# Optimization experiments

Hardware: AMD Instinct MI355X
Metric: run time of the kernel (lower is better)

Reference implementation:

```python
import jax, jax.numpy as jnp
import numpy as np

D = 128
NUM_GATE = 100000
T = 524288
IDX_MAX = 256


def sinusoid_table(n, d):
    # generate_fixed_embedding for indices 0..n-1, vectorized
    pos = jnp.arange(n, dtype=jnp.float32)[:, None]                      # [n,1]
    div = jnp.exp(jnp.arange(0, d, 2, dtype=jnp.float32)
                  * (-jnp.log(jnp.float32(10000.0)) / d))                # [d/2]
    ang = pos * div                                                      # [n,d/2]
    enc = jnp.zeros((n, d), jnp.float32)
    return enc.at[:, 0::2].set(jnp.sin(ang)).at[:, 1::2].set(jnp.cos(ang))


def setup_inputs() -> dict:
    key = jax.random.key(0)
    ks = jax.random.split(key, 10)
    bound = 1.0 / np.sqrt(3 * D)  # torch Linear default init bound
    return {
        "gate_emb": jax.random.normal(ks[0], (NUM_GATE, D), jnp.float32),
        "edge_emb": jax.random.normal(ks[1], (2, D), jnp.float32),
        "W": jax.random.uniform(ks[2], (D, 3 * D), jnp.float32, -bound, bound),
        "b": jax.random.uniform(ks[3], (D,), jnp.float32, -bound, bound),
        "src_idx": jax.random.randint(ks[4], (T,), 0, IDX_MAX, jnp.int32),
        "src_type": jax.random.randint(ks[5], (T,), 0, 4, jnp.int32),
        "rel": jax.random.randint(ks[6], (T,), 0, 2, jnp.int32),
        "dst_idx": jax.random.randint(ks[7], (T,), 0, IDX_MAX, jnp.int32),
        "dst_type": jax.random.randint(ks[8], (T,), 0, 4, jnp.int32),
        "num_input_nodes": IDX_MAX,
        "num_output_nodes": IDX_MAX,
    }


def reference(gate_emb, edge_emb, W, b, src_idx, src_type, rel, dst_idx,
              dst_type, num_input_nodes, num_output_nodes):
    d = gate_emb.shape[1]
    inp_enc = sinusoid_table(num_input_nodes, d)    # [Ni,d]
    out_enc = sinusoid_table(num_output_nodes, d)   # [No,d]
    ni, no, ng = inp_enc.shape[0], out_enc.shape[0], gate_emb.shape[0]
    # one flat table: [input | output | gate | constant(zeros)]
    table = jnp.concatenate(
        [inp_enc, out_enc, gate_emb, jnp.zeros((1, d), gate_emb.dtype)], axis=0)
    offsets = jnp.array([0, ni, ni + no, ni + no + ng], jnp.int32)

    def node_embed(idx, typ):
        # constant nodes (type 3) ignore idx and map to the zero row
        flat = offsets[typ] + jnp.where(typ == 3, 0, idx)
        return table[flat]                           # [T,d]

    src = node_embed(src_idx, src_type)
    dst = node_embed(dst_idx, dst_type)
    r = edge_emb[rel]                                # [T,d]
    x = jnp.concatenate([src, r, dst], axis=-1)      # [T,3d]
    return x @ W.T + b                               # [T,d]
```

## Files before the change

kernel.cpp:

```cpp
#include <hip/hip_runtime.h>
#include <math.h>

#define DD 128
#define NROWS 769
#define T_TOTAL 524288

typedef float vfloat4 __attribute__((ext_vector_type(4)));


#define WT_OFF    0
#define PSRC_OFF  (3 * DD * DD)
#define PDST_OFF  (PSRC_OFF + NROWS * DD)
#define PREL_OFF  (PDST_OFF + NROWS * DD)

__global__ void transposeW(const float* __restrict__ W, float* __restrict__ Wt) {
    int k = blockIdx.x;
    int j = threadIdx.x;
    Wt[0 * DD * DD + k * DD + j] = W[j * 384 + k];
    Wt[1 * DD * DD + k * DD + j] = W[j * 384 + 128 + k];
    Wt[2 * DD * DD + k * DD + j] = W[j * 384 + 256 + k];
}

__global__ __launch_bounds__(DD) void prep(
    const float* __restrict__ gate_emb, const float* __restrict__ edge_emb,
    const float* __restrict__ b, const float* __restrict__ Wt,
    float* __restrict__ Psrc, float* __restrict__ Pdst,
    float* __restrict__ Prel) {
    __shared__ float row[DD];
    int r = blockIdx.x;
    int j = threadIdx.x;

    if (r < NROWS) {
        float v;
        if (r < 512) {
            int p = r & 255;
            int i = j >> 1;
            float div = expf(-logf(10000.0f) * (2.0f * (float)i) / 128.0f);
            float ang = (float)p * div;
            v = (j & 1) ? cosf(ang) : sinf(ang);
        } else if (r < 768) {
            v = gate_emb[(r - 512) * DD + j];
        } else {
            v = 0.0f;
        }
        row[j] = v;
        __syncthreads();
        const float* Ws = Wt;
        const float* Wd = Wt + 2 * DD * DD;
        float s = 0.0f, d = 0.0f;
#pragma unroll 8
        for (int k = 0; k < DD; ++k) {
            float e = row[k];
            s = fmaf(e, Ws[k * DD + j], s);
            d = fmaf(e, Wd[k * DD + j], d);
        }
        Psrc[r * DD + j] = s;
        Pdst[r * DD + j] = d;
    } else {
        int rr = r - NROWS;
        row[j] = edge_emb[rr * DD + j];
        __syncthreads();
        const float* Wr = Wt + 1 * DD * DD;
        float s = b[j];
#pragma unroll 8
        for (int k = 0; k < DD; ++k) s = fmaf(row[k], Wr[k * DD + j], s);
        Prel[rr * DD + j] = s;
    }
}

__global__ __launch_bounds__(256) void gather_add(
    const int* __restrict__ src_idx, const int* __restrict__ src_type,
    const int* __restrict__ rel, const int* __restrict__ dst_idx,
    const int* __restrict__ dst_type,
    const vfloat4* __restrict__ Psrc, const vfloat4* __restrict__ Pdst,
    const vfloat4* __restrict__ Prel, vfloat4* __restrict__ out) {
    __shared__ int spk[64];
    int tid  = threadIdx.x;
    int lane = tid & 31;
    int grp  = tid >> 5;
    int rowBase = blockIdx.x * 64;

    if (tid < 64) {
        int t = rowBase + tid;
        int s = src_type[t], d = dst_type[t];
        int fs = (s == 3) ? 768 : s * 256 + src_idx[t];
        int fd = (d == 3) ? 768 : d * 256 + dst_idx[t];
        spk[tid] = fs | (fd << 10) | (rel[t] << 20);
    }
    vfloat4 rel0 = Prel[lane];
    vfloat4 rel1 = Prel[32 + lane];
    __syncthreads();

    int pk[8];
#pragma unroll
    for (int i = 0; i < 8; ++i) pk[i] = spk[grp + 8 * i];

    vfloat4 a[8], c[8];
#pragma unroll
    for (int i = 0; i < 8; ++i) a[i] = Psrc[(pk[i] & 1023) * 32 + lane];
#pragma unroll
    for (int i = 0; i < 8; ++i) c[i] = Pdst[((pk[i] >> 10) & 1023) * 32 + lane];

#pragma unroll
    for (int i = 0; i < 8; ++i) {
        vfloat4 o = a[i] + c[i] + ((pk[i] >> 20) ? rel1 : rel0);
        __builtin_nontemporal_store(o, &out[(rowBase + grp + 8 * i) * 32 + lane]);
    }
}

extern "C" void kernel_launch(void* const* d_in, const int* in_sizes, int n_in,
                              void* d_out, int out_size, void* d_ws, size_t ws_size,
                              hipStream_t stream) {
    const float* gate_emb = (const float*)d_in[0];
    const float* edge_emb = (const float*)d_in[1];
    const float* W        = (const float*)d_in[2];
    const float* b        = (const float*)d_in[3];
    const int* src_idx    = (const int*)d_in[4];
    const int* src_type   = (const int*)d_in[5];
    const int* rel        = (const int*)d_in[6];
    const int* dst_idx    = (const int*)d_in[7];
    const int* dst_type   = (const int*)d_in[8];

    float* ws   = (float*)d_ws;
    float* Wt   = ws + WT_OFF;
    float* Psrc = ws + PSRC_OFF;
    float* Pdst = ws + PDST_OFF;
    float* Prel = ws + PREL_OFF;

    transposeW<<<DD, DD, 0, stream>>>(W, Wt);
    prep<<<NROWS + 2, DD, 0, stream>>>(gate_emb, edge_emb, b, Wt,
                                       Psrc, Pdst, Prel);
    gather_add<<<T_TOTAL / 64, 256, 0, stream>>>(
        src_idx, src_type, rel, dst_idx, dst_type,
        (const vfloat4*)Psrc, (const vfloat4*)Pdst, (const vfloat4*)Prel,
        (vfloat4*)d_out);
}
```

Before: 338.7 us.

## Precompute packed gather indices in the transpose kernel, drop shared-memory sync

```diff
diff --git a/kernel.cpp b/kernel.cpp
--- a/kernel.cpp
+++ b/kernel.cpp
@@ -6,19 +6,44 @@
 #define T_TOTAL 524288
 
 typedef float vfloat4 __attribute__((ext_vector_type(4)));
+typedef int   vint4   __attribute__((ext_vector_type(4)));
 
 
 #define WT_OFF    0
 #define PSRC_OFF  (3 * DD * DD)
 #define PDST_OFF  (PSRC_OFF + NROWS * DD)
 #define PREL_OFF  (PDST_OFF + NROWS * DD)
+#define PK_OFF    (PREL_OFF + 2 * DD)
 
-__global__ void transposeW(const float* __restrict__ W, float* __restrict__ Wt) {
-    int k = blockIdx.x;
-    int j = threadIdx.x;
-    Wt[0 * DD * DD + k * DD + j] = W[j * 384 + k];
-    Wt[1 * DD * DD + k * DD + j] = W[j * 384 + 128 + k];
-    Wt[2 * DD * DD + k * DD + j] = W[j * 384 + 256 + k];
+__global__ __launch_bounds__(DD) void pre(
+    const float* __restrict__ W, float* __restrict__ Wt,
+    const int* __restrict__ src_idx, const int* __restrict__ src_type,
+    const int* __restrict__ rel, const int* __restrict__ dst_idx,
+    const int* __restrict__ dst_type, int* __restrict__ pk) {
+    int bid = blockIdx.x;
+    int tid = threadIdx.x;
+    if (bid < DD) {
+        int k = bid;
+        int j = tid;
+        Wt[0 * DD * DD + k * DD + j] = W[j * 384 + k];
+        Wt[1 * DD * DD + k * DD + j] = W[j * 384 + 128 + k];
+        Wt[2 * DD * DD + k * DD + j] = W[j * 384 + 256 + k];
+    } else {
+        int t4 = (bid - DD) * DD + tid;
+        vint4 si = ((const vint4*)src_idx)[t4];
+        vint4 st = ((const vint4*)src_type)[t4];
+        vint4 rl = ((const vint4*)rel)[t4];
+        vint4 di = ((const vint4*)dst_idx)[t4];
+        vint4 dt = ((const vint4*)dst_type)[t4];
+        vint4 o;
+#pragma unroll
+        for (int m = 0; m < 4; ++m) {
+            int fs = (st[m] == 3) ? 768 : st[m] * 256 + si[m];
+            int fd = (dt[m] == 3) ? 768 : dt[m] * 256 + di[m];
+            o[m] = fs | (fd << 10) | (rl[m] << 20);
+        }
+        ((vint4*)pk)[t4] = o;
+    }
 }
 
 __global__ __launch_bounds__(DD) void prep(
@@ -69,42 +94,33 @@
 }
 
 __global__ __launch_bounds__(256) void gather_add(
-    const int* __restrict__ src_idx, const int* __restrict__ src_type,
-    const int* __restrict__ rel, const int* __restrict__ dst_idx,
-    const int* __restrict__ dst_type,
+    const int* __restrict__ pk,
     const vfloat4* __restrict__ Psrc, const vfloat4* __restrict__ Pdst,
     const vfloat4* __restrict__ Prel, vfloat4* __restrict__ out) {
-    __shared__ int spk[64];
     int tid  = threadIdx.x;
     int lane = tid & 31;
     int grp  = tid >> 5;
     int rowBase = blockIdx.x * 64;
 
-    if (tid < 64) {
-        int t = rowBase + tid;
-        int s = src_type[t], d = dst_type[t];
-        int fs = (s == 3) ? 768 : s * 256 + src_idx[t];
-        int fd = (d == 3) ? 768 : d * 256 + dst_idx[t];
-        spk[tid] = fs | (fd << 10) | (rel[t] << 20);
-    }
+    vint4 pkA = ((const vint4*)pk)[(rowBase >> 2) + grp * 2];
+    vint4 pkB = ((const vint4*)pk)[(rowBase >> 2) + grp * 2 + 1];
     vfloat4 rel0 = Prel[lane];
     vfloat4 rel1 = Prel[32 + lane];
-    __syncthreads();
 
-    int pk[8];
-#pragma unroll
-    for (int i = 0; i < 8; ++i) pk[i] = spk[grp + 8 * i];
+    int p[8] = {pkA[0], pkA[1], pkA[2], pkA[3],
+                pkB[0], pkB[1], pkB[2], pkB[3]};
 
     vfloat4 a[8], c[8];
 #pragma unroll
-    for (int i = 0; i < 8; ++i) a[i] = Psrc[(pk[i] & 1023) * 32 + lane];
+    for (int i = 0; i < 8; ++i) a[i] = Psrc[(p[i] & 1023) * 32 + lane];
 #pragma unroll
-    for (int i = 0; i < 8; ++i) c[i] = Pdst[((pk[i] >> 10) & 1023) * 32 + lane];
+    for (int i = 0; i < 8; ++i) c[i] = Pdst[((p[i] >> 10) & 1023) * 32 + lane];
 
+    int rowT = rowBase + grp * 8;
 #pragma unroll
     for (int i = 0; i < 8; ++i) {
-        vfloat4 o = a[i] + c[i] + ((pk[i] >> 20) ? rel1 : rel0);
-        __builtin_nontemporal_store(o, &out[(rowBase + grp + 8 * i) * 32 + lane]);
+        vfloat4 o = a[i] + c[i] + ((p[i] >> 20) ? rel1 : rel0);
+        __builtin_nontemporal_store(o, &out[(rowT + i) * 32 + lane]);
     }
 }
 
@@ -126,12 +142,13 @@
     float* Psrc = ws + PSRC_OFF;
     float* Pdst = ws + PDST_OFF;
     float* Prel = ws + PREL_OFF;
+    int*   pk   = (int*)(ws + PK_OFF);
 
-    transposeW<<<DD, DD, 0, stream>>>(W, Wt);
+    pre<<<DD + T_TOTAL / (DD * 4), DD, 0, stream>>>(
+        W, Wt, src_idx, src_type, rel, dst_idx, dst_type, pk);
     prep<<<NROWS + 2, DD, 0, stream>>>(gate_emb, edge_emb, b, Wt,
                                        Psrc, Pdst, Prel);
     gather_add<<<T_TOTAL / 64, 256, 0, stream>>>(
-        src_idx, src_type, rel, dst_idx, dst_type,
-        (const vfloat4*)Psrc, (const vfloat4*)Pdst, (const vfloat4*)Prel,
-        (vfloat4*)d_out);
+        pk, (const vfloat4*)Psrc, (const vfloat4*)Pdst,
+        (const vfloat4*)Prel, (vfloat4*)d_out);
 }
```

New measurement: 319.5 us. 1.06x faster.
